# Kernel tuning notes

Hardware: AMD Instinct MI355X
Metric: run time of the kernel (lower is better)

Reference implementation:

```python
import jax, jax.numpy as jnp
import numpy as np

N_STEPS = 7
N_TERMS = 4


def _sobel_kernel2d():
    dx = jnp.array([[-1.0, 0.0, 1.0], [-2.0, 0.0, 2.0], [-1.0, 0.0, 1.0]], dtype=jnp.float32)
    dy = jnp.array([[-1.0, -2.0, -1.0], [0.0, 0.0, 0.0], [1.0, 2.0, 1.0]], dtype=jnp.float32)
    return 0.125 * jnp.stack([dy, dx, dy, dx], 0)[:, None]  # [4,1,3,3]


def _grid_sample_bilinear(src, sx, sy):
    # src: [N,C,H,W]; sx,sy: [N,H,W] pixel coords (align_corners=False, zeros padding)
    N, C, H, W = src.shape
    x0 = jnp.floor(sx)
    y0 = jnp.floor(sy)
    wx = (sx - x0)[:, None]  # [N,1,H,W]
    wy = (sy - y0)[:, None]
    x0i = x0.astype(jnp.int32)
    y0i = y0.astype(jnp.int32)

    def gather(yi, xi):
        valid = ((xi >= 0) & (xi < W) & (yi >= 0) & (yi < H))
        xc = jnp.clip(xi, 0, W - 1)
        yc = jnp.clip(yi, 0, H - 1)
        v = jax.vmap(lambda im, y, x: im[:, y, x])(src, yc, xc)  # [N,C,H,W]
        return v * valid[:, None].astype(src.dtype)

    v00 = gather(y0i, x0i)
    v01 = gather(y0i, x0i + 1)
    v10 = gather(y0i + 1, x0i)
    v11 = gather(y0i + 1, x0i + 1)
    return (v00 * (1 - wx) * (1 - wy) + v01 * wx * (1 - wy)
            + v10 * (1 - wx) * wy + v11 * wx * wy)


def _transform(src, disp, gy, gx, H, W):
    # new pixel locations; torch normalizes with (size-1) but samples with
    # align_corners=False, net mapping: p -> p*S/(S-1) - 0.5
    py = gy + disp[:, 0]
    px = gx + disp[:, 1]
    sy = py * (H / (H - 1)) - 0.5
    sx = px * (W / (W - 1)) - 0.5
    return _grid_sample_bilinear(src, sx, sy)


def _jacobian2d(vel):
    # replicate-pad then depthwise sobel conv -> [N,2,2,H,W]
    N, _, H, W = vel.shape
    padded = jnp.pad(vel, ((0, 0), (0, 0), (1, 1), (1, 1)), mode='edge')
    jac = jax.lax.conv_general_dilated(
        padded, _sobel_kernel2d(), window_strides=(1, 1), padding='VALID',
        feature_group_count=2, dimension_numbers=('NCHW', 'OIHW', 'NCHW'))
    return jac.reshape(N, 2, 2, H, W)


def _logdet1p(jac, eps):
    # -sum_n (-eps)^n tr(J^n)/n over the 2x2 dims, per pixel -> [N,H,W]
    ld = jnp.zeros(jac.shape[:1] + jac.shape[-2:], dtype=jac.dtype)
    xn = jac
    for n in range(1, N_TERMS + 1):
        if n > 1:
            xn = jnp.einsum('nikhw,nkjhw->nijhw', xn, jac)
        tr = xn[:, 0, 0] + xn[:, 1, 1]
        ld = ld - ((-eps) ** n) * tr / n
    return ld


def _integrate(vel, logdet_jac):
    N, _, H, W = vel.shape
    gy, gx = jnp.meshgrid(jnp.arange(H, dtype=vel.dtype),
                          jnp.arange(W, dtype=vel.dtype), indexing='ij')
    eps = 2.0 ** (-N_STEPS)
    disp = eps * vel
    if logdet_jac:
        ldjac = _logdet1p(_jacobian2d(vel), eps)[:, None]  # [N,1,H,W]
    else:
        ldjac = None
    for _ in range(N_STEPS):
        disp = disp + _transform(disp, disp, gy, gx, H, W)
        if logdet_jac:
            ldjac = ldjac + _transform(ldjac, disp, gy, gx, H, W)
    return disp, ldjac


def setup_inputs() -> dict:
    key = jax.random.key(0)
    vel = jax.random.normal(key, (16, 2, 512, 512), dtype=jnp.float32)
    return {"vel": vel, "logdet_jac": 1}


def reference(vel, logdet_jac):
    return _integrate(vel, bool(logdet_jac))
```

## Files before the change

kernel.cpp:

```cpp
#include <hip/hip_runtime.h>


#define NB 16
#define HH 512
#define WW 512
#define HW (HH * WW)
#define TOT (NB * HW)
#define EPS 0.0078125f
#define DISP_ELEMS (NB * 2 * HW)
#define SC (512.0f / 511.0f)

typedef _Float16 f16;
typedef _Float16 f16x4 __attribute__((ext_vector_type(4)));

struct SampC {
    int yc0, xc0, yc1, xc1;
    float w00, w01, w10, w11;
};

__device__ __forceinline__ SampC make_sampc(float sy, float sx) {
    float fy = floorf(sy), fx = floorf(sx);
    float wy = sy - fy, wx = sx - fx;
    int y0 = (int)fy, x0 = (int)fx;
    int y1 = y0 + 1, x1 = x0 + 1;
    bool xv0 = (unsigned)x0 < (unsigned)WW;
    bool xv1 = (unsigned)x1 < (unsigned)WW;
    bool yv0 = (unsigned)y0 < (unsigned)HH;
    bool yv1 = (unsigned)y1 < (unsigned)HH;
    SampC s;
    s.xc0 = min(max(x0, 0), WW - 1); s.xc1 = min(max(x1, 0), WW - 1);
    s.yc0 = min(max(y0, 0), HH - 1); s.yc1 = min(max(y1, 0), HH - 1);
    float omwx = 1.0f - wx, omwy = 1.0f - wy;
    s.w00 = (xv0 && yv0) ? omwx * omwy : 0.0f;
    s.w01 = (xv1 && yv0) ? wx * omwy   : 0.0f;
    s.w10 = (xv0 && yv1) ? omwx * wy   : 0.0f;
    s.w11 = (xv1 && yv1) ? wx * wy     : 0.0f;
    return s;
}

__device__ __forceinline__ f16x4 step_rec(f16x4 rv, f16x4 g00, f16x4 g01,
                                          f16x4 g10, f16x4 g11, const SampC& s) {
    float d0 = (float)rv.x, d1 = (float)rv.y, l = (float)rv.z;
    float nd0 = d0 + s.w00 * (float)g00.x + s.w01 * (float)g01.x
                   + s.w10 * (float)g10.x + s.w11 * (float)g11.x;
    float nd1 = d1 + s.w00 * (float)g00.y + s.w01 * (float)g01.y
                   + s.w10 * (float)g10.y + s.w11 * (float)g11.y;
    float nl  = l  + s.w00 * (float)g00.z + s.w01 * (float)g01.z
                   + s.w10 * (float)g10.z + s.w11 * (float)g11.z;
    f16x4 w; w.x = (f16)nd0; w.y = (f16)nd1; w.z = (f16)nl; w.w = (f16)0.0f;
    return w;
}

__device__ __forceinline__ int remap_idx() {
    int bid = blockIdx.x;
    int task = ((bid & 7) << 11) | (bid >> 3);
    return task * 256 + threadIdx.x;
}

__device__ __forceinline__ float rnd16(float v) { return (float)(f16)v; }

__global__ void __launch_bounds__(256) init_fused(const float* __restrict__ vel,
                                                  f16x4* __restrict__ rdst) {
    int idx = remap_idx();
    int n = idx >> 18;
    int rem = idx & (HW - 1);
    int y = rem >> 9, x = rem & (WW - 1);

    const float* v0 = vel + (size_t)n * 2 * HW;
    const float* v1 = v0 + HW;

    int ym = max(y - 1, 0), yp = min(y + 1, HH - 1);
    int xm = max(x - 1, 0), xp = min(x + 1, WW - 1);
    int r0 = ym * WW, r1 = y * WW, r2 = yp * WW;

    float A00 = v0[r0 + xm], A01 = v0[r0 + x], A02 = v0[r0 + xp];
    float A10 = v0[r1 + xm], A11 = v0[r1 + x], A12 = v0[r1 + xp];
    float A20 = v0[r2 + xm], A21 = v0[r2 + x], A22 = v0[r2 + xp];
    float B00 = v1[r0 + xm], B01 = v1[r0 + x], B02 = v1[r0 + xp];
    float B10 = v1[r1 + xm], B11 = v1[r1 + x], B12 = v1[r1 + xp];
    float B20 = v1[r2 + xm], B21 = v1[r2 + x], B22 = v1[r2 + xp];

    float a = 0.125f * ((A20 + 2.0f * A21 + A22) - (A00 + 2.0f * A01 + A02));
    float b = 0.125f * ((A02 + 2.0f * A12 + A22) - (A00 + 2.0f * A10 + A20));
    float c = 0.125f * ((B20 + 2.0f * B21 + B22) - (B00 + 2.0f * B01 + B02));
    float d = 0.125f * ((B02 + 2.0f * B12 + B22) - (B00 + 2.0f * B10 + B20));

    float xa = a, xb = b, xc = c, xd = d;
    float ld = EPS * (xa + xd);
    float na = xa * a + xb * c, nb = xa * b + xb * d;
    float nc = xc * a + xd * c, nd = xc * b + xd * d;
    xa = na; xb = nb; xc = nc; xd = nd;
    ld -= (EPS * EPS) * (xa + xd) * 0.5f;
    na = xa * a + xb * c; nb = xa * b + xb * d;
    nc = xc * a + xd * c; nd = xc * b + xd * d;
    xa = na; xb = nb; xc = nc; xd = nd;
    ld += (EPS * EPS * EPS) * (xa + xd) * (1.0f / 3.0f);
    na = xa * a + xb * c;
    nd = xc * b + xd * d;
    ld -= (EPS * EPS * EPS * EPS) * (na + nd) * 0.25f;

    float d0 = rnd16(EPS * A11);
    float d1 = rnd16(EPS * B11);

    float sy = fmaf((float)y + d0, SC, -0.5f);
    float sx = fmaf((float)x + d1, SC, -0.5f);
    SampC s = make_sampc(sy, sx);

    bool rlo = (sy < (float)y);
    bool clo = (sx < (float)x);

    float Ar0c0 = rlo ? A00 : A10, Ar0c1 = rlo ? A01 : A11, Ar0c2 = rlo ? A02 : A12;
    float Ar1c0 = rlo ? A10 : A20, Ar1c1 = rlo ? A11 : A21, Ar1c2 = rlo ? A12 : A22;
    float Br0c0 = rlo ? B00 : B10, Br0c1 = rlo ? B01 : B11, Br0c2 = rlo ? B02 : B12;
    float Br1c0 = rlo ? B10 : B20, Br1c1 = rlo ? B11 : B21, Br1c2 = rlo ? B12 : B22;

    float g00x = rnd16(EPS * (clo ? Ar0c0 : Ar0c1));
    float g01x = rnd16(EPS * (clo ? Ar0c1 : Ar0c2));
    float g10x = rnd16(EPS * (clo ? Ar1c0 : Ar1c1));
    float g11x = rnd16(EPS * (clo ? Ar1c1 : Ar1c2));
    float g00y = rnd16(EPS * (clo ? Br0c0 : Br0c1));
    float g01y = rnd16(EPS * (clo ? Br0c1 : Br0c2));
    float g10y = rnd16(EPS * (clo ? Br1c0 : Br1c1));
    float g11y = rnd16(EPS * (clo ? Br1c1 : Br1c2));

    float nd0 = d0 + s.w00 * g00x + s.w01 * g01x + s.w10 * g10x + s.w11 * g11x;
    float nd1 = d1 + s.w00 * g00y + s.w01 * g01y + s.w10 * g10y + s.w11 * g11y;

    f16x4 rec;
    rec.x = (f16)nd0; rec.y = (f16)nd1; rec.z = (f16)ld; rec.w = (f16)0.0f;
    rdst[(size_t)n * HW + rem] = rec;
}

template <int CW, int CH, int R1, int R2>
__global__ void __launch_bounds__(256) step_pair(const f16x4* __restrict__ rsrc,
                                                 f16x4* __restrict__ rdst) {
    constexpr int MW = CW + 2 * R2, MH = CH + 2 * R2;
    constexpr int EW = CW + 2 * (R1 + R2), EH = CH + 2 * (R1 + R2);
    __shared__ f16x4 IN[EH][EW + 1];
    __shared__ f16x4 MID[MH][MW + 1];

    int b = blockIdx.x;
    int xcd = b & 7, sub = b >> 3;
    constexpr int TPI = (512 / CW) * (512 / CH);
    int img = 2 * xcd + (sub >= TPI ? 1 : 0);
    int tile = (sub >= TPI) ? sub - TPI : sub;
    int tx0 = (tile % (512 / CW)) * CW;
    int ty0 = (tile / (512 / CW)) * CH;

    const f16x4* rp = rsrc + (size_t)img * HW;
    int t = threadIdx.x;

    for (int i = t; i < EH * EW; i += 256) {
        int ey = i / EW, ex = i - ey * EW;
        int iy = min(max(ty0 - (R1 + R2) + ey, 0), HH - 1);
        int ix = min(max(tx0 - (R1 + R2) + ex, 0), WW - 1);
        IN[ey][ex] = rp[iy * WW + ix];
    }
    __syncthreads();

    {
        const int oy = ty0 - (R1 + R2), ox = tx0 - (R1 + R2);
        for (int i = t; i < MH * MW; i += 256) {
            int my = i / MW, mx = i - my * MW;
            int qy = ty0 - R2 + my, qx = tx0 - R2 + mx;
            f16x4 rv = IN[my + R1][mx + R1];
            float sy = fmaf((float)qy + (float)rv.x, SC, -0.5f);
            float sx = fmaf((float)qx + (float)rv.y, SC, -0.5f);
            SampC s = make_sampc(sy, sx);
            f16x4 g00 = IN[s.yc0 - oy][s.xc0 - ox];
            f16x4 g01 = IN[s.yc0 - oy][s.xc1 - ox];
            f16x4 g10 = IN[s.yc1 - oy][s.xc0 - ox];
            f16x4 g11 = IN[s.yc1 - oy][s.xc1 - ox];
            MID[my][mx] = step_rec(rv, g00, g01, g10, g11, s);
        }
    }
    __syncthreads();

    {
        const int oy = ty0 - R2, ox = tx0 - R2;
        f16x4* wp = rdst + (size_t)img * HW;
        for (int i = t; i < CH * CW; i += 256) {
            int cy = i / CW, cx = i - cy * CW;
            int qy = ty0 + cy, qx = tx0 + cx;
            f16x4 rv = MID[cy + R2][cx + R2];
            float sy = fmaf((float)qy + (float)rv.x, SC, -0.5f);
            float sx = fmaf((float)qx + (float)rv.y, SC, -0.5f);
            SampC s = make_sampc(sy, sx);
            f16x4 g00 = MID[s.yc0 - oy][s.xc0 - ox];
            f16x4 g01 = MID[s.yc0 - oy][s.xc1 - ox];
            f16x4 g10 = MID[s.yc1 - oy][s.xc0 - ox];
            f16x4 g11 = MID[s.yc1 - oy][s.xc1 - ox];
            wp[qy * WW + qx] = step_rec(rv, g00, g01, g10, g11, s);
        }
    }
}

__global__ void __launch_bounds__(256) step_final(const f16x4* __restrict__ rsrc,
                                                  float* __restrict__ doutp,
                                                  float* __restrict__ loutp) {
    int idx = remap_idx();
    int n = idx >> 18;
    int rem = idx & (HW - 1);
    int y = rem >> 9, x = rem & (WW - 1);

    const f16x4* rp = rsrc + (size_t)n * HW;

    f16x4 rv = rp[rem];
    float d0 = (float)rv.x, d1 = (float)rv.y, l = (float)rv.z;

    float sy = fmaf((float)y + d0, SC, -0.5f);
    float sx = fmaf((float)x + d1, SC, -0.5f);
    SampC s = make_sampc(sy, sx);

    f16x4 g00 = rp[s.yc0 * WW + s.xc0], g01 = rp[s.yc0 * WW + s.xc1];
    f16x4 g10 = rp[s.yc1 * WW + s.xc0], g11 = rp[s.yc1 * WW + s.xc1];

    float nl = l + s.w00 * (float)g00.z + s.w01 * (float)g01.z
                 + s.w10 * (float)g10.z + s.w11 * (float)g11.z;

    float* pd = doutp + (size_t)n * 2 * HW;
    pd[rem]      = d0;
    pd[HW + rem] = d1;
    loutp[(size_t)n * HW + rem] = nl;
}

extern "C" void kernel_launch(void* const* d_in, const int* in_sizes, int n_in,
                              void* d_out, int out_size, void* d_ws, size_t ws_size,
                              hipStream_t stream) {
    const float* vel = (const float*)d_in[0];
    float* out = (float*)d_out;

    f16x4* rA = (f16x4*)d_out;
    f16x4* rB = (f16x4*)d_ws;

    dim3 block(256);

    init_fused<<<dim3(TOT / 256), block, 0, stream>>>(vel, rA);
    step_pair<32, 32, 2, 2><<<dim3(4096), block, 0, stream>>>(rA, rB);
    step_pair<32, 32, 2, 2><<<dim3(4096), block, 0, stream>>>(rB, rA);
    step_pair<32, 32, 3, 4><<<dim3(4096), block, 0, stream>>>(rA, rB);
    step_final<<<dim3(TOT / 256), block, 0, stream>>>(rB, out, out + DISP_ELEMS);
}
```

Before: 120.6 us.

## Fuse init with two steps and final three steps into tiled kernels

Restructures the pipeline from five launches into three: the init kernel (Jacobian log-det plus first step) is fused with two more integration steps in shared memory, a pair kernel does two steps, and the last kernel performs three steps plus the final logdet sample and float output write. This cuts global round trips of the f16x4 state and launch count, at the cost of larger halos with redundant recomputation and big shared-memory footprints. Shared buffers are aliased between stages, and intermediate results are staged in registers before being written back, to save LDS.

```diff
diff --git a/kernel.cpp b/kernel.cpp
--- a/kernel.cpp
+++ b/kernel.cpp
@@ -12,6 +12,7 @@
 
 typedef _Float16 f16;
 typedef _Float16 f16x4 __attribute__((ext_vector_type(4)));
+typedef float f32x2 __attribute__((ext_vector_type(2)));
 
 struct SampC {
     int yc0, xc0, yc1, xc1;
@@ -51,138 +52,116 @@
     return w;
 }
 
-__device__ __forceinline__ int remap_idx() {
-    int bid = blockIdx.x;
-    int task = ((bid & 7) << 11) | (bid >> 3);
-    return task * 256 + threadIdx.x;
-}
-
 __device__ __forceinline__ float rnd16(float v) { return (float)(f16)v; }
 
-__global__ void __launch_bounds__(256) init_fused(const float* __restrict__ vel,
-                                                  f16x4* __restrict__ rdst) {
-    int idx = remap_idx();
-    int n = idx >> 18;
-    int rem = idx & (HW - 1);
-    int y = rem >> 9, x = rem & (WW - 1);
-
-    const float* v0 = vel + (size_t)n * 2 * HW;
+__device__ __forceinline__ void tile_map(int& img, int& ty0, int& tx0) {
+    int bidx = blockIdx.x;
+    int xcd = bidx & 7, sub = bidx >> 3;
+    img = 2 * xcd + (sub >= 256 ? 1 : 0);
+    int tile = sub & 255;
+    tx0 = (tile & 15) << 5;
+    ty0 = (tile >> 4) << 5;
+}
+
+__global__ void __launch_bounds__(256, 4) p1_fused(const float* __restrict__ vel,
+                                                   f16x4* __restrict__ rdst) {
+    __shared__ __align__(16) char smemV[42 * 43 * 8];
+    __shared__ __align__(16) f16x4 REC[40][41];
+    f32x2 (*VEL)[43] = (f32x2 (*)[43])smemV;
+    f16x4 (*MID)[37] = (f16x4 (*)[37])smemV;
+
+    int img, ty0, tx0;
+    tile_map(img, ty0, tx0);
+    int t = threadIdx.x;
+
+    const float* v0 = vel + (size_t)img * 2 * HW;
     const float* v1 = v0 + HW;
 
-    int ym = max(y - 1, 0), yp = min(y + 1, HH - 1);
-    int xm = max(x - 1, 0), xp = min(x + 1, WW - 1);
-    int r0 = ym * WW, r1 = y * WW, r2 = yp * WW;
-
-    float A00 = v0[r0 + xm], A01 = v0[r0 + x], A02 = v0[r0 + xp];
-    float A10 = v0[r1 + xm], A11 = v0[r1 + x], A12 = v0[r1 + xp];
-    float A20 = v0[r2 + xm], A21 = v0[r2 + x], A22 = v0[r2 + xp];
-    float B00 = v1[r0 + xm], B01 = v1[r0 + x], B02 = v1[r0 + xp];
-    float B10 = v1[r1 + xm], B11 = v1[r1 + x], B12 = v1[r1 + xp];
-    float B20 = v1[r2 + xm], B21 = v1[r2 + x], B22 = v1[r2 + xp];
-
-    float a = 0.125f * ((A20 + 2.0f * A21 + A22) - (A00 + 2.0f * A01 + A02));
-    float b = 0.125f * ((A02 + 2.0f * A12 + A22) - (A00 + 2.0f * A10 + A20));
-    float c = 0.125f * ((B20 + 2.0f * B21 + B22) - (B00 + 2.0f * B01 + B02));
-    float d = 0.125f * ((B02 + 2.0f * B12 + B22) - (B00 + 2.0f * B10 + B20));
-
-    float xa = a, xb = b, xc = c, xd = d;
-    float ld = EPS * (xa + xd);
-    float na = xa * a + xb * c, nb = xa * b + xb * d;
-    float nc = xc * a + xd * c, nd = xc * b + xd * d;
-    xa = na; xb = nb; xc = nc; xd = nd;
-    ld -= (EPS * EPS) * (xa + xd) * 0.5f;
-    na = xa * a + xb * c; nb = xa * b + xb * d;
-    nc = xc * a + xd * c; nd = xc * b + xd * d;
-    xa = na; xb = nb; xc = nc; xd = nd;
-    ld += (EPS * EPS * EPS) * (xa + xd) * (1.0f / 3.0f);
-    na = xa * a + xb * c;
-    nd = xc * b + xd * d;
-    ld -= (EPS * EPS * EPS * EPS) * (na + nd) * 0.25f;
-
-    float d0 = rnd16(EPS * A11);
-    float d1 = rnd16(EPS * B11);
-
-    float sy = fmaf((float)y + d0, SC, -0.5f);
-    float sx = fmaf((float)x + d1, SC, -0.5f);
-    SampC s = make_sampc(sy, sx);
-
-    bool rlo = (sy < (float)y);
-    bool clo = (sx < (float)x);
-
-    float Ar0c0 = rlo ? A00 : A10, Ar0c1 = rlo ? A01 : A11, Ar0c2 = rlo ? A02 : A12;
-    float Ar1c0 = rlo ? A10 : A20, Ar1c1 = rlo ? A11 : A21, Ar1c2 = rlo ? A12 : A22;
-    float Br0c0 = rlo ? B00 : B10, Br0c1 = rlo ? B01 : B11, Br0c2 = rlo ? B02 : B12;
-    float Br1c0 = rlo ? B10 : B20, Br1c1 = rlo ? B11 : B21, Br1c2 = rlo ? B12 : B22;
-
-    float g00x = rnd16(EPS * (clo ? Ar0c0 : Ar0c1));
-    float g01x = rnd16(EPS * (clo ? Ar0c1 : Ar0c2));
-    float g10x = rnd16(EPS * (clo ? Ar1c0 : Ar1c1));
-    float g11x = rnd16(EPS * (clo ? Ar1c1 : Ar1c2));
-    float g00y = rnd16(EPS * (clo ? Br0c0 : Br0c1));
-    float g01y = rnd16(EPS * (clo ? Br0c1 : Br0c2));
-    float g10y = rnd16(EPS * (clo ? Br1c0 : Br1c1));
-    float g11y = rnd16(EPS * (clo ? Br1c1 : Br1c2));
-
-    float nd0 = d0 + s.w00 * g00x + s.w01 * g01x + s.w10 * g10x + s.w11 * g11x;
-    float nd1 = d1 + s.w00 * g00y + s.w01 * g01y + s.w10 * g10y + s.w11 * g11y;
-
-    f16x4 rec;
-    rec.x = (f16)nd0; rec.y = (f16)nd1; rec.z = (f16)ld; rec.w = (f16)0.0f;
-    rdst[(size_t)n * HW + rem] = rec;
-}
-
-template <int CW, int CH, int R1, int R2>
-__global__ void __launch_bounds__(256) step_pair(const f16x4* __restrict__ rsrc,
-                                                 f16x4* __restrict__ rdst) {
-    constexpr int MW = CW + 2 * R2, MH = CH + 2 * R2;
-    constexpr int EW = CW + 2 * (R1 + R2), EH = CH + 2 * (R1 + R2);
-    __shared__ f16x4 IN[EH][EW + 1];
-    __shared__ f16x4 MID[MH][MW + 1];
-
-    int b = blockIdx.x;
-    int xcd = b & 7, sub = b >> 3;
-    constexpr int TPI = (512 / CW) * (512 / CH);
-    int img = 2 * xcd + (sub >= TPI ? 1 : 0);
-    int tile = (sub >= TPI) ? sub - TPI : sub;
-    int tx0 = (tile % (512 / CW)) * CW;
-    int ty0 = (tile / (512 / CW)) * CH;
-
-    const f16x4* rp = rsrc + (size_t)img * HW;
-    int t = threadIdx.x;
-
-    for (int i = t; i < EH * EW; i += 256) {
-        int ey = i / EW, ex = i - ey * EW;
-        int iy = min(max(ty0 - (R1 + R2) + ey, 0), HH - 1);
-        int ix = min(max(tx0 - (R1 + R2) + ex, 0), WW - 1);
-        IN[ey][ex] = rp[iy * WW + ix];
-    }
-    __syncthreads();
-
-    {
-        const int oy = ty0 - (R1 + R2), ox = tx0 - (R1 + R2);
-        for (int i = t; i < MH * MW; i += 256) {
-            int my = i / MW, mx = i - my * MW;
-            int qy = ty0 - R2 + my, qx = tx0 - R2 + mx;
-            f16x4 rv = IN[my + R1][mx + R1];
+    for (int i = t; i < 42 * 42; i += 256) {
+        int ey = i / 42, ex = i - ey * 42;
+        int gy = min(max(ty0 - 5 + ey, 0), HH - 1);
+        int gx = min(max(tx0 - 5 + ex, 0), WW - 1);
+        f32x2 v; v.x = v0[gy * WW + gx]; v.y = v1[gy * WW + gx];
+        VEL[ey][ex] = v;
+    }
+    __syncthreads();
+
+    {
+        const int oy = ty0 - 5, ox = tx0 - 5;
+        for (int i = t; i < 1600; i += 256) {
+            int ry = i / 40, rx = i - ry * 40;
+            int qy = ty0 - 4 + ry, qx = tx0 - 4 + rx;
+            f32x2 w00 = VEL[ry][rx],     w01 = VEL[ry][rx + 1],     w02 = VEL[ry][rx + 2];
+            f32x2 w10 = VEL[ry + 1][rx], w11 = VEL[ry + 1][rx + 1], w12 = VEL[ry + 1][rx + 2];
+            f32x2 w20 = VEL[ry + 2][rx], w21 = VEL[ry + 2][rx + 1], w22 = VEL[ry + 2][rx + 2];
+
+            float a = 0.125f * ((w20.x + 2.0f * w21.x + w22.x) - (w00.x + 2.0f * w01.x + w02.x));
+            float b = 0.125f * ((w02.x + 2.0f * w12.x + w22.x) - (w00.x + 2.0f * w10.x + w20.x));
+            float c = 0.125f * ((w20.y + 2.0f * w21.y + w22.y) - (w00.y + 2.0f * w01.y + w02.y));
+            float d = 0.125f * ((w02.y + 2.0f * w12.y + w22.y) - (w00.y + 2.0f * w10.y + w20.y));
+
+            float xa = a, xb = b, xc = c, xd = d;
+            float ld = EPS * (xa + xd);
+            float na = xa * a + xb * c, nb = xa * b + xb * d;
+            float nc = xc * a + xd * c, nd = xc * b + xd * d;
+            xa = na; xb = nb; xc = nc; xd = nd;
+            ld -= (EPS * EPS) * (xa + xd) * 0.5f;
+            na = xa * a + xb * c; nb = xa * b + xb * d;
+            nc = xc * a + xd * c; nd = xc * b + xd * d;
+            xa = na; xb = nb; xc = nc; xd = nd;
+            ld += (EPS * EPS * EPS) * (xa + xd) * (1.0f / 3.0f);
+            na = xa * a + xb * c;
+            nd = xc * b + xd * d;
+            ld -= (EPS * EPS * EPS * EPS) * (na + nd) * 0.25f;
+
+            float d0 = rnd16(EPS * w11.x);
+            float d1 = rnd16(EPS * w11.y);
+
+            float sy = fmaf((float)qy + d0, SC, -0.5f);
+            float sx = fmaf((float)qx + d1, SC, -0.5f);
+            SampC s = make_sampc(sy, sx);
+
+            f32x2 c00 = VEL[s.yc0 - oy][s.xc0 - ox];
+            f32x2 c01 = VEL[s.yc0 - oy][s.xc1 - ox];
+            f32x2 c10 = VEL[s.yc1 - oy][s.xc0 - ox];
+            f32x2 c11 = VEL[s.yc1 - oy][s.xc1 - ox];
+
+            float nd0 = d0 + s.w00 * rnd16(EPS * c00.x) + s.w01 * rnd16(EPS * c01.x)
+                           + s.w10 * rnd16(EPS * c10.x) + s.w11 * rnd16(EPS * c11.x);
+            float nd1 = d1 + s.w00 * rnd16(EPS * c00.y) + s.w01 * rnd16(EPS * c01.y)
+                           + s.w10 * rnd16(EPS * c10.y) + s.w11 * rnd16(EPS * c11.y);
+
+            f16x4 rec; rec.x = (f16)nd0; rec.y = (f16)nd1; rec.z = (f16)ld; rec.w = (f16)0.0f;
+            REC[ry][rx] = rec;
+        }
+    }
+    __syncthreads();
+
+    {
+        const int oy = ty0 - 4, ox = tx0 - 4;
+        for (int i = t; i < 1296; i += 256) {
+            int my = i / 36, mx = i - my * 36;
+            int qy = ty0 - 2 + my, qx = tx0 - 2 + mx;
+            f16x4 rv = REC[my + 2][mx + 2];
             float sy = fmaf((float)qy + (float)rv.x, SC, -0.5f);
             float sx = fmaf((float)qx + (float)rv.y, SC, -0.5f);
             SampC s = make_sampc(sy, sx);
-            f16x4 g00 = IN[s.yc0 - oy][s.xc0 - ox];
-            f16x4 g01 = IN[s.yc0 - oy][s.xc1 - ox];
-            f16x4 g10 = IN[s.yc1 - oy][s.xc0 - ox];
-            f16x4 g11 = IN[s.yc1 - oy][s.xc1 - ox];
+            f16x4 g00 = REC[s.yc0 - oy][s.xc0 - ox];
+            f16x4 g01 = REC[s.yc0 - oy][s.xc1 - ox];
+            f16x4 g10 = REC[s.yc1 - oy][s.xc0 - ox];
+            f16x4 g11 = REC[s.yc1 - oy][s.xc1 - ox];
             MID[my][mx] = step_rec(rv, g00, g01, g10, g11, s);
         }
     }
     __syncthreads();
 
     {
-        const int oy = ty0 - R2, ox = tx0 - R2;
+        const int oy = ty0 - 2, ox = tx0 - 2;
         f16x4* wp = rdst + (size_t)img * HW;
-        for (int i = t; i < CH * CW; i += 256) {
-            int cy = i / CW, cx = i - cy * CW;
+        for (int i = t; i < 1024; i += 256) {
+            int cy = i >> 5, cx = i & 31;
             int qy = ty0 + cy, qx = tx0 + cx;
-            f16x4 rv = MID[cy + R2][cx + R2];
+            f16x4 rv = MID[cy + 2][cx + 2];
             float sy = fmaf((float)qy + (float)rv.x, SC, -0.5f);
             float sx = fmaf((float)qx + (float)rv.y, SC, -0.5f);
             SampC s = make_sampc(sy, sx);
@@ -195,33 +174,175 @@
     }
 }
 
-__global__ void __launch_bounds__(256) step_final(const f16x4* __restrict__ rsrc,
-                                                  float* __restrict__ doutp,
-                                                  float* __restrict__ loutp) {
-    int idx = remap_idx();
-    int n = idx >> 18;
-    int rem = idx & (HW - 1);
-    int y = rem >> 9, x = rem & (WW - 1);
-
-    const f16x4* rp = rsrc + (size_t)n * HW;
-
-    f16x4 rv = rp[rem];
-    float d0 = (float)rv.x, d1 = (float)rv.y, l = (float)rv.z;
-
-    float sy = fmaf((float)y + d0, SC, -0.5f);
-    float sx = fmaf((float)x + d1, SC, -0.5f);
-    SampC s = make_sampc(sy, sx);
-
-    f16x4 g00 = rp[s.yc0 * WW + s.xc0], g01 = rp[s.yc0 * WW + s.xc1];
-    f16x4 g10 = rp[s.yc1 * WW + s.xc0], g11 = rp[s.yc1 * WW + s.xc1];
-
-    float nl = l + s.w00 * (float)g00.z + s.w01 * (float)g01.z
-                 + s.w10 * (float)g10.z + s.w11 * (float)g11.z;
-
-    float* pd = doutp + (size_t)n * 2 * HW;
-    pd[rem]      = d0;
-    pd[HW + rem] = d1;
-    loutp[(size_t)n * HW + rem] = nl;
+__global__ void __launch_bounds__(256, 6) p2_pair(const f16x4* __restrict__ rsrc,
+                                                  f16x4* __restrict__ rdst) {
+    __shared__ __align__(16) char smem[40 * 41 * 8];
+    f16x4 (*IN)[41]  = (f16x4 (*)[41])smem;
+    f16x4 (*MID)[37] = (f16x4 (*)[37])smem;
+
+    int img, ty0, tx0;
+    tile_map(img, ty0, tx0);
+    int t = threadIdx.x;
+    const f16x4* rp = rsrc + (size_t)img * HW;
+
+    for (int i = t; i < 1600; i += 256) {
+        int ey = i / 40, ex = i - ey * 40;
+        int gy = min(max(ty0 - 4 + ey, 0), HH - 1);
+        int gx = min(max(tx0 - 4 + ex, 0), WW - 1);
+        IN[ey][ex] = rp[gy * WW + gx];
+    }
+    __syncthreads();
+
+    f16x4 st[6];
+    {
+        const int oy = ty0 - 4, ox = tx0 - 4;
+#pragma unroll
+        for (int k = 0; k < 6; ++k) {
+            int i = t + (k << 8);
+            if (i < 1296) {
+                int my = i / 36, mx = i - my * 36;
+                int qy = ty0 - 2 + my, qx = tx0 - 2 + mx;
+                f16x4 rv = IN[my + 2][mx + 2];
+                float sy = fmaf((float)qy + (float)rv.x, SC, -0.5f);
+                float sx = fmaf((float)qx + (float)rv.y, SC, -0.5f);
+                SampC s = make_sampc(sy, sx);
+                f16x4 g00 = IN[s.yc0 - oy][s.xc0 - ox];
+                f16x4 g01 = IN[s.yc0 - oy][s.xc1 - ox];
+                f16x4 g10 = IN[s.yc1 - oy][s.xc0 - ox];
+                f16x4 g11 = IN[s.yc1 - oy][s.xc1 - ox];
+                st[k] = step_rec(rv, g00, g01, g10, g11, s);
+            }
+        }
+    }
+    __syncthreads();
+#pragma unroll
+    for (int k = 0; k < 6; ++k) {
+        int i = t + (k << 8);
+        if (i < 1296) MID[i / 36][i - (i / 36) * 36] = st[k];
+    }
+    __syncthreads();
+
+    {
+        const int oy = ty0 - 2, ox = tx0 - 2;
+        f16x4* wp = rdst + (size_t)img * HW;
+        for (int i = t; i < 1024; i += 256) {
+            int cy = i >> 5, cx = i & 31;
+            int qy = ty0 + cy, qx = tx0 + cx;
+            f16x4 rv = MID[cy + 2][cx + 2];
+            float sy = fmaf((float)qy + (float)rv.x, SC, -0.5f);
+            float sx = fmaf((float)qx + (float)rv.y, SC, -0.5f);
+            SampC s = make_sampc(sy, sx);
+            f16x4 g00 = MID[s.yc0 - oy][s.xc0 - ox];
+            f16x4 g01 = MID[s.yc0 - oy][s.xc1 - ox];
+            f16x4 g10 = MID[s.yc1 - oy][s.xc0 - ox];
+            f16x4 g11 = MID[s.yc1 - oy][s.xc1 - ox];
+            wp[qy * WW + qx] = step_rec(rv, g00, g01, g10, g11, s);
+        }
+    }
+}
+
+__global__ void __launch_bounds__(256, 4) p3_fused(const f16x4* __restrict__ rsrc,
+                                                   float* __restrict__ doutp,
+                                                   float* __restrict__ loutp) {
+    __shared__ __align__(16) char smem[62 * 63 * 8];
+    f16x4 (*IN)[63] = (f16x4 (*)[63])smem;
+    f16x4 (*M1)[57] = (f16x4 (*)[57])smem;
+    f16x4 (*M2)[49] = (f16x4 (*)[49])smem;
+
+    int img, ty0, tx0;
+    tile_map(img, ty0, tx0);
+    int t = threadIdx.x;
+    const f16x4* rp = rsrc + (size_t)img * HW;
+
+    for (int i = t; i < 62 * 62; i += 256) {
+        int ey = i / 62, ex = i - ey * 62;
+        int gy = min(max(ty0 - 15 + ey, 0), HH - 1);
+        int gx = min(max(tx0 - 15 + ex, 0), WW - 1);
+        IN[ey][ex] = rp[gy * WW + gx];
+    }
+    __syncthreads();
+
+    f16x4 st1[13];
+    {
+        const int oy = ty0 - 15, ox = tx0 - 15;
+#pragma unroll
+        for (int k = 0; k < 13; ++k) {
+            int i = t + (k << 8);
+            if (i < 3136) {
+                int my = i / 56, mx = i - my * 56;
+                int qy = ty0 - 12 + my, qx = tx0 - 12 + mx;
+                f16x4 rv = IN[my + 3][mx + 3];
+                float sy = fmaf((float)qy + (float)rv.x, SC, -0.5f);
+                float sx = fmaf((float)qx + (float)rv.y, SC, -0.5f);
+                SampC s = make_sampc(sy, sx);
+                f16x4 g00 = IN[s.yc0 - oy][s.xc0 - ox];
+                f16x4 g01 = IN[s.yc0 - oy][s.xc1 - ox];
+                f16x4 g10 = IN[s.yc1 - oy][s.xc0 - ox];
+                f16x4 g11 = IN[s.yc1 - oy][s.xc1 - ox];
+                st1[k] = step_rec(rv, g00, g01, g10, g11, s);
+            }
+        }
+    }
+    __syncthreads();
+#pragma unroll
+    for (int k = 0; k < 13; ++k) {
+        int i = t + (k << 8);
+        if (i < 3136) M1[i / 56][i - (i / 56) * 56] = st1[k];
+    }
+    __syncthreads();
+
+    f16x4 st2[9];
+    {
+        const int oy = ty0 - 12, ox = tx0 - 12;
+#pragma unroll
+        for (int k = 0; k < 9; ++k) {
+            int i = t + (k << 8);
+            if (i < 2304) {
+                int my = i / 48, mx = i - my * 48;
+                int qy = ty0 - 8 + my, qx = tx0 - 8 + mx;
+                f16x4 rv = M1[my + 4][mx + 4];
+                float sy = fmaf((float)qy + (float)rv.x, SC, -0.5f);
+                float sx = fmaf((float)qx + (float)rv.y, SC, -0.5f);
+                SampC s = make_sampc(sy, sx);
+                f16x4 g00 = M1[s.yc0 - oy][s.xc0 - ox];
+                f16x4 g01 = M1[s.yc0 - oy][s.xc1 - ox];
+                f16x4 g10 = M1[s.yc1 - oy][s.xc0 - ox];
+                f16x4 g11 = M1[s.yc1 - oy][s.xc1 - ox];
+                st2[k] = step_rec(rv, g00, g01, g10, g11, s);
+            }
+        }
+    }
+    __syncthreads();
+#pragma unroll
+    for (int k = 0; k < 9; ++k) {
+        int i = t + (k << 8);
+        if (i < 2304) M2[i / 48][i - (i / 48) * 48] = st2[k];
+    }
+    __syncthreads();
+
+    {
+        const int oy = ty0 - 8, ox = tx0 - 8;
+        float* pd = doutp + (size_t)img * 2 * HW;
+        float* pl = loutp + (size_t)img * HW;
+        for (int i = t; i < 1024; i += 256) {
+            int cy = i >> 5, cx = i & 31;
+            int qy = ty0 + cy, qx = tx0 + cx;
+            f16x4 rv = M2[cy + 8][cx + 8];
+            float d0 = (float)rv.x, d1 = (float)rv.y, l = (float)rv.z;
+            float sy = fmaf((float)qy + d0, SC, -0.5f);
+            float sx = fmaf((float)qx + d1, SC, -0.5f);
+            SampC s = make_sampc(sy, sx);
+            f16x4 g00 = M2[s.yc0 - oy][s.xc0 - ox];
+            f16x4 g01 = M2[s.yc0 - oy][s.xc1 - ox];
+            f16x4 g10 = M2[s.yc1 - oy][s.xc0 - ox];
+            f16x4 g11 = M2[s.yc1 - oy][s.xc1 - ox];
+            float nl = l + s.w00 * (float)g00.z + s.w01 * (float)g01.z
+                         + s.w10 * (float)g10.z + s.w11 * (float)g11.z;
+            pd[qy * WW + qx]      = d0;
+            pd[HW + qy * WW + qx] = d1;
+            pl[qy * WW + qx]      = nl;
+        }
+    }
 }
 
 extern "C" void kernel_launch(void* const* d_in, const int* in_sizes, int n_in,
@@ -230,14 +351,12 @@
     const float* vel = (const float*)d_in[0];
     float* out = (float*)d_out;
 
-    f16x4* rA = (f16x4*)d_out;
-    f16x4* rB = (f16x4*)d_ws;
-
-    dim3 block(256);
-
-    init_fused<<<dim3(TOT / 256), block, 0, stream>>>(vel, rA);
-    step_pair<32, 32, 2, 2><<<dim3(4096), block, 0, stream>>>(rA, rB);
-    step_pair<32, 32, 2, 2><<<dim3(4096), block, 0, stream>>>(rB, rA);
-    step_pair<32, 32, 3, 4><<<dim3(4096), block, 0, stream>>>(rA, rB);
-    step_final<<<dim3(TOT / 256), block, 0, stream>>>(rB, out, out + DISP_ELEMS);
-}
+    f16x4* rX1 = (f16x4*)d_out;
+    f16x4* rX2 = (f16x4*)d_ws;
+
+    dim3 block(256), grid(4096);
+
+    p1_fused<<<grid, block, 0, stream>>>(vel, rX1);
+    p2_pair<<<grid, block, 0, stream>>>(rX1, rX2);
+    p3_fused<<<grid, block, 0, stream>>>(rX2, out, out + DISP_ELEMS);
+}
```

Measured after the change: 150.8 us. 25.0% more time.

## Fuse three integration steps per tiled kernel instead of two

Applied to the files above, without the earlier changes.

Replaces the two-step shared-memory tile kernel with a three-step version, so the six middle steps take two launches instead of three. This removes one full global read/write pass of the f16x4 state. In exchange each tile loads a wider halo and does more redundant boundary computation. The last stage's buffer reuses the input tile's shared memory to limit LDS use, and launch bounds now request 4 blocks per CU.

```diff
diff --git a/kernel.cpp b/kernel.cpp
--- a/kernel.cpp
+++ b/kernel.cpp
@@ -51,13 +51,22 @@
     return w;
 }
 
+__device__ __forceinline__ float rnd16(float v) { return (float)(f16)v; }
+
+__device__ __forceinline__ void tile_map(int& img, int& ty0, int& tx0) {
+    int bidx = blockIdx.x;
+    int xcd = bidx & 7, sub = bidx >> 3;
+    img = 2 * xcd + (sub >= 256 ? 1 : 0);
+    int tile = sub & 255;
+    tx0 = (tile & 15) << 5;
+    ty0 = (tile >> 4) << 5;
+}
+
 __device__ __forceinline__ int remap_idx() {
     int bid = blockIdx.x;
     int task = ((bid & 7) << 11) | (bid >> 3);
     return task * 256 + threadIdx.x;
 }
-
-__device__ __forceinline__ float rnd16(float v) { return (float)(f16)v; }
 
 __global__ void __launch_bounds__(256) init_fused(const float* __restrict__ vel,
                                                   f16x4* __restrict__ rdst) {
@@ -131,38 +140,34 @@
     rdst[(size_t)n * HW + rem] = rec;
 }
 
-template <int CW, int CH, int R1, int R2>
-__global__ void __launch_bounds__(256) step_pair(const f16x4* __restrict__ rsrc,
-                                                 f16x4* __restrict__ rdst) {
-    constexpr int MW = CW + 2 * R2, MH = CH + 2 * R2;
-    constexpr int EW = CW + 2 * (R1 + R2), EH = CH + 2 * (R1 + R2);
-    __shared__ f16x4 IN[EH][EW + 1];
-    __shared__ f16x4 MID[MH][MW + 1];
-
-    int b = blockIdx.x;
-    int xcd = b & 7, sub = b >> 3;
-    constexpr int TPI = (512 / CW) * (512 / CH);
-    int img = 2 * xcd + (sub >= TPI ? 1 : 0);
-    int tile = (sub >= TPI) ? sub - TPI : sub;
-    int tx0 = (tile % (512 / CW)) * CW;
-    int ty0 = (tile / (512 / CW)) * CH;
-
+template <int R1, int R2, int R3>
+__global__ void __launch_bounds__(256, 4) step_triple(const f16x4* __restrict__ rsrc,
+                                                      f16x4* __restrict__ rdst) {
+    constexpr int M2d = 32 + 2 * R3;
+    constexpr int M1d = 32 + 2 * (R2 + R3);
+    constexpr int Ed  = 32 + 2 * (R1 + R2 + R3);
+    __shared__ __align__(16) f16x4 IN[Ed][Ed + 1];
+    __shared__ __align__(16) f16x4 M1[M1d][M1d + 1];
+    f16x4 (*M2)[M2d + 1] = (f16x4 (*)[M2d + 1])&IN[0][0];
+
+    int img, ty0, tx0;
+    tile_map(img, ty0, tx0);
+    int t = threadIdx.x;
     const f16x4* rp = rsrc + (size_t)img * HW;
-    int t = threadIdx.x;
-
-    for (int i = t; i < EH * EW; i += 256) {
-        int ey = i / EW, ex = i - ey * EW;
-        int iy = min(max(ty0 - (R1 + R2) + ey, 0), HH - 1);
-        int ix = min(max(tx0 - (R1 + R2) + ex, 0), WW - 1);
-        IN[ey][ex] = rp[iy * WW + ix];
+
+    for (int i = t; i < Ed * Ed; i += 256) {
+        int ey = i / Ed, ex = i - ey * Ed;
+        int gy = min(max(ty0 - (R1 + R2 + R3) + ey, 0), HH - 1);
+        int gx = min(max(tx0 - (R1 + R2 + R3) + ex, 0), WW - 1);
+        IN[ey][ex] = rp[gy * WW + gx];
     }
     __syncthreads();
 
     {
-        const int oy = ty0 - (R1 + R2), ox = tx0 - (R1 + R2);
-        for (int i = t; i < MH * MW; i += 256) {
-            int my = i / MW, mx = i - my * MW;
-            int qy = ty0 - R2 + my, qx = tx0 - R2 + mx;
+        const int oy = ty0 - (R1 + R2 + R3), ox = tx0 - (R1 + R2 + R3);
+        for (int i = t; i < M1d * M1d; i += 256) {
+            int my = i / M1d, mx = i - my * M1d;
+            int qy = ty0 - (R2 + R3) + my, qx = tx0 - (R2 + R3) + mx;
             f16x4 rv = IN[my + R1][mx + R1];
             float sy = fmaf((float)qy + (float)rv.x, SC, -0.5f);
             float sx = fmaf((float)qx + (float)rv.y, SC, -0.5f);
@@ -171,25 +176,43 @@
             f16x4 g01 = IN[s.yc0 - oy][s.xc1 - ox];
             f16x4 g10 = IN[s.yc1 - oy][s.xc0 - ox];
             f16x4 g11 = IN[s.yc1 - oy][s.xc1 - ox];
-            MID[my][mx] = step_rec(rv, g00, g01, g10, g11, s);
+            M1[my][mx] = step_rec(rv, g00, g01, g10, g11, s);
         }
     }
     __syncthreads();
 
     {
-        const int oy = ty0 - R2, ox = tx0 - R2;
-        f16x4* wp = rdst + (size_t)img * HW;
-        for (int i = t; i < CH * CW; i += 256) {
-            int cy = i / CW, cx = i - cy * CW;
-            int qy = ty0 + cy, qx = tx0 + cx;
-            f16x4 rv = MID[cy + R2][cx + R2];
+        const int oy = ty0 - (R2 + R3), ox = tx0 - (R2 + R3);
+        for (int i = t; i < M2d * M2d; i += 256) {
+            int my = i / M2d, mx = i - my * M2d;
+            int qy = ty0 - R3 + my, qx = tx0 - R3 + mx;
+            f16x4 rv = M1[my + R2][mx + R2];
             float sy = fmaf((float)qy + (float)rv.x, SC, -0.5f);
             float sx = fmaf((float)qx + (float)rv.y, SC, -0.5f);
             SampC s = make_sampc(sy, sx);
-            f16x4 g00 = MID[s.yc0 - oy][s.xc0 - ox];
-            f16x4 g01 = MID[s.yc0 - oy][s.xc1 - ox];
-            f16x4 g10 = MID[s.yc1 - oy][s.xc0 - ox];
-            f16x4 g11 = MID[s.yc1 - oy][s.xc1 - ox];
+            f16x4 g00 = M1[s.yc0 - oy][s.xc0 - ox];
+            f16x4 g01 = M1[s.yc0 - oy][s.xc1 - ox];
+            f16x4 g10 = M1[s.yc1 - oy][s.xc0 - ox];
+            f16x4 g11 = M1[s.yc1 - oy][s.xc1 - ox];
+            M2[my][mx] = step_rec(rv, g00, g01, g10, g11, s);
+        }
+    }
+    __syncthreads();
+
+    {
+        const int oy = ty0 - R3, ox = tx0 - R3;
+        f16x4* wp = rdst + (size_t)img * HW;
+        for (int i = t; i < 1024; i += 256) {
+            int cy = i >> 5, cx = i & 31;
+            int qy = ty0 + cy, qx = tx0 + cx;
+            f16x4 rv = M2[cy + R3][cx + R3];
+            float sy = fmaf((float)qy + (float)rv.x, SC, -0.5f);
+            float sx = fmaf((float)qx + (float)rv.y, SC, -0.5f);
+            SampC s = make_sampc(sy, sx);
+            f16x4 g00 = M2[s.yc0 - oy][s.xc0 - ox];
+            f16x4 g01 = M2[s.yc0 - oy][s.xc1 - ox];
+            f16x4 g10 = M2[s.yc1 - oy][s.xc0 - ox];
+            f16x4 g11 = M2[s.yc1 - oy][s.xc1 - ox];
             wp[qy * WW + qx] = step_rec(rv, g00, g01, g10, g11, s);
         }
     }
@@ -230,14 +253,13 @@
     const float* vel = (const float*)d_in[0];
     float* out = (float*)d_out;
 
-    f16x4* rA = (f16x4*)d_out;
-    f16x4* rB = (f16x4*)d_ws;
-
-    dim3 block(256);
-
-    init_fused<<<dim3(TOT / 256), block, 0, stream>>>(vel, rA);
-    step_pair<32, 32, 2, 2><<<dim3(4096), block, 0, stream>>>(rA, rB);
-    step_pair<32, 32, 2, 2><<<dim3(4096), block, 0, stream>>>(rB, rA);
-    step_pair<32, 32, 3, 4><<<dim3(4096), block, 0, stream>>>(rA, rB);
-    step_final<<<dim3(TOT / 256), block, 0, stream>>>(rB, out, out + DISP_ELEMS);
-}
+    f16x4* rWS  = (f16x4*)d_ws;
+    f16x4* rOUT = (f16x4*)d_out;
+
+    dim3 block(256), gridT(4096), gridS(TOT / 256);
+
+    init_fused<<<gridS, block, 0, stream>>>(vel, rWS);
+    step_triple<2, 2, 2><<<gridT, block, 0, stream>>>(rWS, rOUT);
+    step_triple<2, 3, 4><<<gridT, block, 0, stream>>>(rOUT, rWS);
+    step_final<<<gridS, block, 0, stream>>>(rWS, out, out + DISP_ELEMS);
+}
```

Measured after the change: 125.8 us, median of 2. 1.04x slower.
